# Optimization experiments

Hardware: AMD Instinct MI355X
Metric: run time of the kernel (lower is better)

Reference implementation:

```python
import jax, jax.numpy as jnp
import numpy as np

N_NODES = 50000
N_EDGES = 800000
D_IN = 128
D_HID = 128
N_CLASSES = 10


def setup_inputs() -> dict:
    key = jax.random.key(0)
    ks = jax.random.split(key, 8)
    x = jax.random.normal(ks[0], (N_NODES, D_IN), dtype=jnp.float32)
    edge_index = jax.random.randint(ks[1], (2, N_EDGES), 0, N_NODES, dtype=jnp.int64)
    s = 1.0 / np.sqrt(D_IN)
    W1 = jax.random.uniform(ks[2], (D_IN, D_HID), jnp.float32, -s, s)
    b1 = jnp.zeros((D_HID,), jnp.float32)
    W2 = jax.random.uniform(ks[3], (D_HID, D_HID), jnp.float32, -s, s)
    b2 = jnp.zeros((D_HID,), jnp.float32)
    sl = 1.0 / np.sqrt(D_HID)
    Wl = jax.random.uniform(ks[4], (D_HID, N_CLASSES), jnp.float32, -sl, sl)
    bl = jax.random.uniform(ks[5], (N_CLASSES,), jnp.float32, -sl, sl)
    return {"x": x, "edge_index": edge_index, "W1": W1, "b1": b1,
            "W2": W2, "b2": b2, "Wl": Wl, "bl": bl}


def gcn_conv(x, src, dst, W, b, n_nodes):
    # PyG GCNConv: add self-loops, symmetric normalization, gather-scatter aggregate
    h = x @ W                                             # [N, D_out]
    loop = jnp.arange(n_nodes, dtype=src.dtype)
    src2 = jnp.concatenate([src, loop])                   # [E+N]
    dst2 = jnp.concatenate([dst, loop])
    deg = jax.ops.segment_sum(jnp.ones_like(dst2, dtype=h.dtype), dst2,
                              num_segments=n_nodes)       # in-degree incl. self-loop
    dinv = jnp.where(deg > 0, jax.lax.rsqrt(deg), 0.0)
    norm = dinv[src2] * dinv[dst2]                        # [E+N]
    msgs = h[src2] * norm[:, None]                        # gather + scale  [E+N, D_out]
    out = jax.ops.segment_sum(msgs, dst2, num_segments=n_nodes)  # scatter-add
    return out + b


def reference(x, edge_index, W1, b1, W2, b2, Wl, bl):
    src, dst = edge_index[0], edge_index[1]
    n = x.shape[0]
    h = jax.nn.relu(gcn_conv(x, src, dst, W1, b1, n))     # dropout is identity in eval
    h = jax.nn.relu(gcn_conv(h, src, dst, W2, b2, n))
    logits = h @ Wl + bl                                  # [N, C]
    return jax.nn.log_softmax(logits, axis=1)
```

## Files before the change

kernel.cpp:

```cpp
#include <hip/hip_runtime.h>
#include <hip/hip_bf16.h>

#define D 128
#define NCLS 10

typedef short bf16x8 __attribute__((ext_vector_type(8)));
typedef float f32x4 __attribute__((ext_vector_type(4)));

static __device__ __forceinline__ float relu(float x){ return fmaxf(x, 0.0f); }
static __device__ __forceinline__ float bf_lo(unsigned v){ return __uint_as_float(v << 16); }
static __device__ __forceinline__ float bf_hi(unsigned v){ return __uint_as_float(v & 0xffff0000u); }
static __device__ __forceinline__ ushort bf16u(float f){
  __hip_bfloat16 h = __float2bfloat16(f);
  return *reinterpret_cast<ushort*>(&h);
}
static __device__ __forceinline__ unsigned relu_bf2(unsigned v){
  if (v & 0x00008000u) v &= 0xFFFF0000u;
  if (v & 0x80000000u) v &= 0x0000FFFFu;
  return v;
}

__global__ __launch_bounds__(256) void k_init(int* __restrict__ counts2, int nz,
                                              const float* __restrict__ W1,
                                              const float* __restrict__ W2,
                                              ushort* __restrict__ Wt1,
                                              ushort* __restrict__ Wt2){
  const int nzb = (nz + 255) >> 8;
  const int b = blockIdx.x;
  if (b < nzb){
    int i = b*256 + threadIdx.x;
    if (i < nz) counts2[i] = 0;
  } else {
    int i = (b - nzb)*256 + threadIdx.x;
    int sel = i >> 14;
    int rem = i & 16383;
    int k = rem >> 7, n = rem & 127;
    const float* Ws = sel ? W2 : W1;
    ushort* Wd = sel ? Wt2 : Wt1;
    Wd[n*128 + k] = bf16u(Ws[rem]);
  }
}

__global__ __launch_bounds__(256) void k_hist(const int* __restrict__ dst,
                                              int* __restrict__ counts, int E){
  int i = blockIdx.x*256 + threadIdx.x;
  int e0 = 2*i;
  if (e0 + 1 < E){
    int2 d = ((const int2*)dst)[i];
    atomicAdd(counts + d.x, 1);
    atomicAdd(counts + d.y, 1);
  } else if (e0 < E){
    atomicAdd(counts + dst[e0], 1);
  }
}

__global__ __launch_bounds__(256) void k_scan1(const int* __restrict__ counts,
                                               int2* __restrict__ rowPtr2,
                                               int* __restrict__ bsum,
                                               float* __restrict__ dinv, int n){
  const int i = blockIdx.x*256 + threadIdx.x;
  const int lane = threadIdx.x & 63;
  const int wid  = threadIdx.x >> 6;
  int v = (i < n) ? counts[i] : 0;
  if (i < n) dinv[i] = rsqrtf((float)(v + 1));
  int s = v;
  #pragma unroll
  for (int off = 1; off < 64; off <<= 1){
    int u = __shfl_up(s, off, 64);
    if (lane >= off) s += u;
  }
  __shared__ int ws[4];
  if (lane == 63) ws[wid] = s;
  __syncthreads();
  int add = 0;
  if (wid >= 1) add += ws[0];
  if (wid >= 2) add += ws[1];
  if (wid >= 3) add += ws[2];
  int incl = s + add;
  if (i < n) rowPtr2[i] = make_int2(incl - v, incl);
  if (threadIdx.x == 255) bsum[blockIdx.x] = incl;
}

__global__ __launch_bounds__(256) void k_scan2(int* __restrict__ bsum, int nb){
  const int t = threadIdx.x;
  const int lane = t & 63;
  const int wid  = t >> 6;
  int v = (t < nb) ? bsum[t] : 0;
  int s = v;
  #pragma unroll
  for (int off = 1; off < 64; off <<= 1){
    int u = __shfl_up(s, off, 64);
    if (lane >= off) s += u;
  }
  __shared__ int ws[4];
  if (lane == 63) ws[wid] = s;
  __syncthreads();
  int add = 0;
  if (wid >= 1) add += ws[0];
  if (wid >= 2) add += ws[1];
  if (wid >= 3) add += ws[2];
  int incl = s + add;
  if (t < nb) bsum[t] = incl - v;
}

__global__ __launch_bounds__(256) void k_scatter(const int* __restrict__ src,
                                                 const int* __restrict__ dst,
                                                 const int2* __restrict__ rowPtr2,
                                                 const int* __restrict__ bsum,
                                                 const float* __restrict__ dinv,
                                                 int* __restrict__ cursor,
                                                 int2* __restrict__ edat, int E){
  int i = blockIdx.x*256 + threadIdx.x;
  if (i >= E) return;
  int d = dst[i];
  int s = src[i];
  int pos = rowPtr2[d].x + bsum[d >> 8] + atomicAdd(cursor + d, 1);
  edat[pos] = make_int2(s, __float_as_int(dinv[s]));
}

template<bool BF16IN, bool RELU>
__global__ __launch_bounds__(256) void k_gemm_mfma(const void* __restrict__ Av,
                                                   const ushort* __restrict__ Wt,
                                                   __hip_bfloat16* __restrict__ C,
                                                   int M){
  __shared__ ushort sA[64*136];
  __shared__ ushort sW[128*136];
  const int tid = threadIdx.x;
  const int row0 = blockIdx.x * 64;
  const int rowsHere = (M - row0 >= 64) ? 64 : (M - row0);

  {
    const uint4* Wt4 = (const uint4*)Wt;
    for (int i = tid; i < 2048; i += 256){
      int r = i >> 4, c = i & 15;
      uint4 v = Wt4[i];
      *((uint4*)(sW + r*136 + c*8)) = v;
    }
  }
  if (BF16IN){
    const uint4* A4 = (const uint4*)((const ushort*)Av + (size_t)row0 * D);
    for (int i = tid; i < 64*16; i += 256){
      int r = i >> 4, c = i & 15;
      uint4 v = make_uint4(0,0,0,0);
      if (r < rowsHere) v = A4[i];
      if (RELU){ v.x = relu_bf2(v.x); v.y = relu_bf2(v.y);
                 v.z = relu_bf2(v.z); v.w = relu_bf2(v.w); }
      *((uint4*)(sA + r*136 + c*8)) = v;
    }
  } else {
    const float4* A4 = (const float4*)Av + (size_t)row0 * 32;
    for (int i = tid; i < 64*32; i += 256){
      int r = i >> 5, c = i & 31;
      float4 v = make_float4(0.f,0.f,0.f,0.f);
      if (r < rowsHere) v = A4[i];
      if (RELU){ v.x=relu(v.x); v.y=relu(v.y); v.z=relu(v.z); v.w=relu(v.w); }
      ushort4 p;
      p.x = bf16u(v.x); p.y = bf16u(v.y); p.z = bf16u(v.z); p.w = bf16u(v.w);
      *((ushort4*)(sA + r*136 + c*4)) = p;
    }
  }
  __syncthreads();

  const int wid  = tid >> 6;
  const int lane = tid & 63;
  const int fr = lane & 15;
  const int fq = lane >> 4;
  const ushort* aBase = sA + (wid*16 + fr)*136 + fq*8;
  const ushort* wBase = sW + fr*136 + fq*8;

  f32x4 acc0 = {0.f,0.f,0.f,0.f}, acc1 = acc0, acc2 = acc0, acc3 = acc0;
  f32x4 acc4 = acc0, acc5 = acc0, acc6 = acc0, acc7 = acc0;
  #pragma unroll
  for (int ks = 0; ks < 4; ++ks){
    bf16x8 a = *(const bf16x8*)(aBase + ks*32);
    bf16x8 b;
    b = *(const bf16x8*)(wBase + 0*16*136 + ks*32);
    acc0 = __builtin_amdgcn_mfma_f32_16x16x32_bf16(a, b, acc0, 0, 0, 0);
    b = *(const bf16x8*)(wBase + 1*16*136 + ks*32);
    acc1 = __builtin_amdgcn_mfma_f32_16x16x32_bf16(a, b, acc1, 0, 0, 0);
    b = *(const bf16x8*)(wBase + 2*16*136 + ks*32);
    acc2 = __builtin_amdgcn_mfma_f32_16x16x32_bf16(a, b, acc2, 0, 0, 0);
    b = *(const bf16x8*)(wBase + 3*16*136 + ks*32);
    acc3 = __builtin_amdgcn_mfma_f32_16x16x32_bf16(a, b, acc3, 0, 0, 0);
    b = *(const bf16x8*)(wBase + 4*16*136 + ks*32);
    acc4 = __builtin_amdgcn_mfma_f32_16x16x32_bf16(a, b, acc4, 0, 0, 0);
    b = *(const bf16x8*)(wBase + 5*16*136 + ks*32);
    acc5 = __builtin_amdgcn_mfma_f32_16x16x32_bf16(a, b, acc5, 0, 0, 0);
    b = *(const bf16x8*)(wBase + 6*16*136 + ks*32);
    acc6 = __builtin_amdgcn_mfma_f32_16x16x32_bf16(a, b, acc6, 0, 0, 0);
    b = *(const bf16x8*)(wBase + 7*16*136 + ks*32);
    acc7 = __builtin_amdgcn_mfma_f32_16x16x32_bf16(a, b, acc7, 0, 0, 0);
  }

  const int rbase = row0 + wid*16 + fq*4;
  #pragma unroll
  for (int r = 0; r < 4; ++r){
    int row = rbase + r;
    if (row < M){
      __hip_bfloat16* crow = C + (size_t)row*D + fr;
      crow[0*16]  = __float2bfloat16(acc0[r]);
      crow[1*16]  = __float2bfloat16(acc1[r]);
      crow[2*16]  = __float2bfloat16(acc2[r]);
      crow[3*16]  = __float2bfloat16(acc3[r]);
      crow[4*16]  = __float2bfloat16(acc4[r]);
      crow[5*16]  = __float2bfloat16(acc5[r]);
      crow[6*16]  = __float2bfloat16(acc6[r]);
      crow[7*16]  = __float2bfloat16(acc7[r]);
    }
  }
}

#define AGG_CORE_BF16                                                          \
  const int grp = lane >> 4;                                                   \
  const int q   = lane & 15;                                                   \
  float dn = dinv[node];                                                       \
  float4 aA0 = make_float4(0,0,0,0), aB0 = aA0, aA1 = aA0, aB1 = aA0;          \
  int2 be = rowPtr2[node];                                                     \
  int bs = bsum[node >> 8];                                                    \
  int beg = be.x + bs, end = be.y + bs;                                        \
  for (int j = beg; j < end; j += 64){                                         \
    int rem = end - j;                                                         \
    int cnt = (rem < 64) ? rem : 64;                                           \
    int2 ed = make_int2(0, 0);                                                 \
    if (lane < cnt) ed = edat[j + lane];                                       \
    int T = (((cnt + 3) >> 2) + 1) & ~1;                                       \
    for (int t = 0; t < T; t += 2){                                            \
      _Pragma("unroll")                                                        \
      for (int u = 0; u < 2; ++u){                                             \
        int e = 4*(t+u) + grp;                                                 \
        int sb = __shfl(ed.x, e);                                              \
        float nb = __uint_as_float((unsigned)__shfl(ed.y, e)) * dn;            \
        uint4 hv = ((const uint4*)(h + (size_t)sb*D))[q];                      \
        float4& cA = u ? aA1 : aA0;                                            \
        float4& cB = u ? aB1 : aB0;                                            \
        cA.x += bf_lo(hv.x)*nb; cA.y += bf_hi(hv.x)*nb;                        \
        cA.z += bf_lo(hv.y)*nb; cA.w += bf_hi(hv.y)*nb;                        \
        cB.x += bf_lo(hv.z)*nb; cB.y += bf_hi(hv.z)*nb;                        \
        cB.z += bf_lo(hv.w)*nb; cB.w += bf_hi(hv.w)*nb;                        \
      }                                                                        \
    }                                                                          \
  }                                                                            \
  float4 rA, rB;                                                               \
  rA.x=aA0.x+aA1.x; rA.y=aA0.y+aA1.y; rA.z=aA0.z+aA1.z; rA.w=aA0.w+aA1.w;      \
  rB.x=aB0.x+aB1.x; rB.y=aB0.y+aB1.y; rB.z=aB0.z+aB1.z; rB.w=aB0.w+aB1.w;      \
  rA.x += __shfl_xor(rA.x,16,64); rA.y += __shfl_xor(rA.y,16,64);              \
  rA.z += __shfl_xor(rA.z,16,64); rA.w += __shfl_xor(rA.w,16,64);              \
  rB.x += __shfl_xor(rB.x,16,64); rB.y += __shfl_xor(rB.y,16,64);              \
  rB.z += __shfl_xor(rB.z,16,64); rB.w += __shfl_xor(rB.w,16,64);              \
  rA.x += __shfl_xor(rA.x,32,64); rA.y += __shfl_xor(rA.y,32,64);              \
  rA.z += __shfl_xor(rA.z,32,64); rA.w += __shfl_xor(rA.w,32,64);              \
  rB.x += __shfl_xor(rB.x,32,64); rB.y += __shfl_xor(rB.y,32,64);              \
  rB.z += __shfl_xor(rB.z,32,64); rB.w += __shfl_xor(rB.w,32,64);

__global__ __launch_bounds__(256) void k_agg_csr(const ushort* __restrict__ h,
                                                 const int2* __restrict__ rowPtr2,
                                                 const int* __restrict__ bsum,
                                                 const int2* __restrict__ edat,
                                                 const float* __restrict__ dinv,
                                                 const float* __restrict__ b,
                                                 ushort* __restrict__ out, int n){
  int gid = blockIdx.x*256 + threadIdx.x;
  int node = gid >> 6;
  int lane = gid & 63;
  if (node >= n) return;
  AGG_CORE_BF16
  if (grp != 0) return;
  uint4 hs = ((const uint4*)(h + (size_t)node*D))[q];
  float sl = dn * dn;
  float4 bA = ((const float4*)b)[2*q];
  float4 bB = ((const float4*)b)[2*q + 1];
  float r[8];
  r[0] = rA.x + bf_lo(hs.x)*sl + bA.x;
  r[1] = rA.y + bf_hi(hs.x)*sl + bA.y;
  r[2] = rA.z + bf_lo(hs.y)*sl + bA.z;
  r[3] = rA.w + bf_hi(hs.y)*sl + bA.w;
  r[4] = rB.x + bf_lo(hs.z)*sl + bB.x;
  r[5] = rB.y + bf_hi(hs.z)*sl + bB.y;
  r[6] = rB.z + bf_lo(hs.w)*sl + bB.z;
  r[7] = rB.w + bf_hi(hs.w)*sl + bB.w;
  union Pack { uint4 u; __hip_bfloat16 b[8]; } p;
  #pragma unroll
  for (int i = 0; i < 8; ++i) p.b[i] = __float2bfloat16(r[i]);
  ((uint4*)(out + (size_t)node*D))[q] = p.u;
}

__global__ __launch_bounds__(256) void k_agg_head(const ushort* __restrict__ h,
                                                  const int2* __restrict__ rowPtr2,
                                                  const int* __restrict__ bsum,
                                                  const int2* __restrict__ edat,
                                                  const float* __restrict__ dinv,
                                                  const float* __restrict__ b,
                                                  const float* __restrict__ Wl,
                                                  const float* __restrict__ bl,
                                                  float* __restrict__ out, int n){
  int gid = blockIdx.x*256 + threadIdx.x;
  int node = gid >> 6;
  int lane = gid & 63;
  if (node >= n) return;
  AGG_CORE_BF16
  if (grp != 0) return;
  uint4 hs = ((const uint4*)(h + (size_t)node*D))[q];
  float sl = dn * dn;
  float4 bA = ((const float4*)b)[2*q];
  float4 bB = ((const float4*)b)[2*q + 1];
  float r[8];
  r[0] = relu(rA.x + bf_lo(hs.x)*sl + bA.x);
  r[1] = relu(rA.y + bf_hi(hs.x)*sl + bA.y);
  r[2] = relu(rA.z + bf_lo(hs.y)*sl + bA.z);
  r[3] = relu(rA.w + bf_hi(hs.y)*sl + bA.w);
  r[4] = relu(rB.x + bf_lo(hs.z)*sl + bB.x);
  r[5] = relu(rB.y + bf_hi(hs.z)*sl + bB.y);
  r[6] = relu(rB.z + bf_lo(hs.w)*sl + bB.z);
  r[7] = relu(rB.w + bf_hi(hs.w)*sl + bB.w);
  float lacc[NCLS];
  #pragma unroll
  for (int c = 0; c < NCLS; ++c){
    float a = 0.f;
    #pragma unroll
    for (int i = 0; i < 8; ++i) a += r[i] * Wl[(8*q + i)*NCLS + c];
    lacc[c] = a;
  }
  #pragma unroll
  for (int c = 0; c < NCLS; ++c){
    #pragma unroll
    for (int off = 8; off >= 1; off >>= 1)
      lacc[c] += __shfl_xor(lacc[c], off, 16);
    lacc[c] += bl[c];
  }
  float m = lacc[0];
  #pragma unroll
  for (int c = 1; c < NCLS; ++c) m = fmaxf(m, lacc[c]);
  float se = 0.f;
  #pragma unroll
  for (int c = 0; c < NCLS; ++c) se += expf(lacc[c] - m);
  float lse = m + logf(se);
  if (q < NCLS){
    float v = lacc[0];
    #pragma unroll
    for (int c = 1; c < NCLS; ++c) if (q == c) v = lacc[c];
    out[(size_t)node*NCLS + q] = v - lse;
  }
}

extern "C" void kernel_launch(void* const* d_in, const int* in_sizes, int n_in,
                              void* d_out, int out_size, void* d_ws, size_t ws_size,
                              hipStream_t stream){
  const float* x  = (const float*)d_in[0];
  const int*   ei = (const int*)d_in[1];
  const float* W1 = (const float*)d_in[2];
  const float* b1 = (const float*)d_in[3];
  const float* W2 = (const float*)d_in[4];
  const float* b2 = (const float*)d_in[5];
  const float* Wl = (const float*)d_in[6];
  const float* bl = (const float*)d_in[7];
  float* out = (float*)d_out;

  const int N = in_sizes[0] / D;
  const int E = in_sizes[1] / 2;
  const int* src = ei;
  const int* dst = ei + E;

  char* ws = (char*)d_ws;
  size_t off = 0;
  ushort* h1    = (ushort*)(ws + off); off += (size_t)N*D*2;
  ushort* g1    = (ushort*)(ws + off); off += (size_t)N*D*2;
  ushort* h2    = (ushort*)(ws + off); off += (size_t)N*D*2;
  ushort* Wt1   = (ushort*)(ws + off); off += (size_t)128*128*2;
  ushort* Wt2   = (ushort*)(ws + off); off += (size_t)128*128*2;
  int*   counts = (int*)(ws + off);    off += (size_t)N*4;
  int*   cursor = (int*)(ws + off);    off += (size_t)N*4;
  int2*  rowPtr2= (int2*)(ws + off);   off += (size_t)N*8;
  float* dinv   = (float*)(ws + off);  off += (size_t)N*4;
  int*   bsum   = (int*)(ws + off);    off += (size_t)256*4;
  int2*  edat   = (int2*)(ws + off);   off += (size_t)E*8;

  const int nbN   = (N + 255)/256;
  const int nb2N  = (2*N + 255)/256;
  const int nbE   = (E + 255)/256;
  const int nbE2  = (E/2 + 255)/256;
  const int initB = nb2N + 128;
  const int gemmB = (N + 63)/64;
  const int aggB  = (N + 3)/4;

  k_init<<<initB, 256, 0, stream>>>(counts, 2*N, W1, W2, Wt1, Wt2);
  k_hist<<<nbE2, 256, 0, stream>>>(dst, counts, E);
  k_scan1<<<nbN, 256, 0, stream>>>(counts, rowPtr2, bsum, dinv, N);
  k_scan2<<<1, 256, 0, stream>>>(bsum, nbN);
  k_scatter<<<nbE, 256, 0, stream>>>(src, dst, rowPtr2, bsum, dinv, cursor, edat, E);

  k_gemm_mfma<false,false><<<gemmB, 256, 0, stream>>>(x, Wt1, (__hip_bfloat16*)h1, N);
  k_agg_csr<<<aggB, 256, 0, stream>>>(h1, rowPtr2, bsum, edat, dinv, b1, g1, N);

  k_gemm_mfma<true,true><<<gemmB, 256, 0, stream>>>(g1, Wt2, (__hip_bfloat16*)h2, N);
  k_agg_head<<<aggB, 256, 0, stream>>>(h2, rowPtr2, bsum, edat, dinv, b2, Wl, bl, out, N);
}
```

Before: 207.5 us.

## Stage gathered neighbor rows into LDS via global_load_lds in aggregation

```diff
diff --git a/kernel.cpp b/kernel.cpp
--- a/kernel.cpp
+++ b/kernel.cpp
@@ -6,6 +6,12 @@
 
 typedef short bf16x8 __attribute__((ext_vector_type(8)));
 typedef float f32x4 __attribute__((ext_vector_type(4)));
+
+typedef __attribute__((address_space(1))) const unsigned int gas_u32;
+typedef __attribute__((address_space(3))) unsigned int las_u32;
+static __device__ __forceinline__ void gload16(const ushort* g, ushort* l){
+  __builtin_amdgcn_global_load_lds((gas_u32*)g, (las_u32*)l, 16, 0, 0);
+}
 
 static __device__ __forceinline__ float relu(float x){ return fmaxf(x, 0.0f); }
 static __device__ __forceinline__ float bf_lo(unsigned v){ return __uint_as_float(v << 16); }
@@ -210,47 +216,47 @@
   }
 }
 
-#define AGG_CORE_BF16                                                          \
-  const int grp = lane >> 4;                                                   \
-  const int q   = lane & 15;                                                   \
+#define AGG_CORE_STAGED                                                        \
+  const int wv   = threadIdx.x >> 6;                                           \
+  const int grp  = lane >> 4;                                                  \
+  const int q    = lane & 15;                                                  \
+  ushort* rowsW = sRows + wv*(32*128);                                         \
+  float*  normW = sNorm + wv*32;                                               \
   float dn = dinv[node];                                                       \
-  float4 aA0 = make_float4(0,0,0,0), aB0 = aA0, aA1 = aA0, aB1 = aA0;          \
+  float accx = 0.f, accy = 0.f;                                                \
   int2 be = rowPtr2[node];                                                     \
   int bs = bsum[node >> 8];                                                    \
   int beg = be.x + bs, end = be.y + bs;                                        \
-  for (int j = beg; j < end; j += 64){                                         \
+  for (int j = beg; j < end; j += 32){                                         \
     int rem = end - j;                                                         \
-    int cnt = (rem < 64) ? rem : 64;                                           \
+    int cnt = (rem < 32) ? rem : 32;                                           \
     int2 ed = make_int2(0, 0);                                                 \
-    if (lane < cnt) ed = edat[j + lane];                                       \
-    int T = (((cnt + 3) >> 2) + 1) & ~1;                                       \
-    for (int t = 0; t < T; t += 2){                                            \
+    float nf = 0.f;                                                            \
+    if (lane < cnt){                                                           \
+      ed = edat[j + lane];                                                     \
+      nf = __uint_as_float((unsigned)ed.y) * dn;                               \
+    }                                                                          \
+    if (lane < 32) normW[lane] = nf;                                           \
+    _Pragma("unroll")                                                          \
+    for (int i = 0; i < 8; ++i){                                               \
+      int e = i*4 + grp;                                                       \
+      e = (e < cnt) ? e : (cnt - 1);                                           \
+      int sb = __shfl(ed.x, e, 64);                                            \
+      gload16(h + ((size_t)sb << 7) + q*8, rowsW + i*512);                     \
+    }                                                                          \
+    asm volatile("s_waitcnt vmcnt(0)" ::: "memory");                           \
+    int T = (cnt + 3) >> 2;                                                    \
+    for (int t = 0; t < T; ++t){                                               \
       _Pragma("unroll")                                                        \
-      for (int u = 0; u < 2; ++u){                                             \
-        int e = 4*(t+u) + grp;                                                 \
-        int sb = __shfl(ed.x, e);                                              \
-        float nb = __uint_as_float((unsigned)__shfl(ed.y, e)) * dn;            \
-        uint4 hv = ((const uint4*)(h + (size_t)sb*D))[q];                      \
-        float4& cA = u ? aA1 : aA0;                                            \
-        float4& cB = u ? aB1 : aB0;                                            \
-        cA.x += bf_lo(hv.x)*nb; cA.y += bf_hi(hv.x)*nb;                        \
-        cA.z += bf_lo(hv.y)*nb; cA.w += bf_hi(hv.y)*nb;                        \
-        cB.x += bf_lo(hv.z)*nb; cB.y += bf_hi(hv.z)*nb;                        \
-        cB.z += bf_lo(hv.w)*nb; cB.w += bf_hi(hv.w)*nb;                        \
+      for (int u = 0; u < 4; ++u){                                             \
+        int k = t*4 + u;                                                       \
+        float nb = normW[k];                                                   \
+        unsigned hv = *(const unsigned*)(rowsW + k*128 + lane*2);              \
+        accx += bf_lo(hv)*nb;                                                  \
+        accy += bf_hi(hv)*nb;                                                  \
       }                                                                        \
     }                                                                          \
-  }                                                                            \
-  float4 rA, rB;                                                               \
-  rA.x=aA0.x+aA1.x; rA.y=aA0.y+aA1.y; rA.z=aA0.z+aA1.z; rA.w=aA0.w+aA1.w;      \
-  rB.x=aB0.x+aB1.x; rB.y=aB0.y+aB1.y; rB.z=aB0.z+aB1.z; rB.w=aB0.w+aB1.w;      \
-  rA.x += __shfl_xor(rA.x,16,64); rA.y += __shfl_xor(rA.y,16,64);              \
-  rA.z += __shfl_xor(rA.z,16,64); rA.w += __shfl_xor(rA.w,16,64);              \
-  rB.x += __shfl_xor(rB.x,16,64); rB.y += __shfl_xor(rB.y,16,64);              \
-  rB.z += __shfl_xor(rB.z,16,64); rB.w += __shfl_xor(rB.w,16,64);              \
-  rA.x += __shfl_xor(rA.x,32,64); rA.y += __shfl_xor(rA.y,32,64);              \
-  rA.z += __shfl_xor(rA.z,32,64); rA.w += __shfl_xor(rA.w,32,64);              \
-  rB.x += __shfl_xor(rB.x,32,64); rB.y += __shfl_xor(rB.y,32,64);              \
-  rB.z += __shfl_xor(rB.z,32,64); rB.w += __shfl_xor(rB.w,32,64);
+  }
 
 __global__ __launch_bounds__(256) void k_agg_csr(const ushort* __restrict__ h,
                                                  const int2* __restrict__ rowPtr2,
@@ -259,29 +265,19 @@
                                                  const float* __restrict__ dinv,
                                                  const float* __restrict__ b,
                                                  ushort* __restrict__ out, int n){
-  int gid = blockIdx.x*256 + threadIdx.x;
-  int node = gid >> 6;
-  int lane = gid & 63;
+  __shared__ ushort sRows[4*32*128];
+  __shared__ float  sNorm[4*32];
+  int node = blockIdx.x*4 + (threadIdx.x >> 6);
+  int lane = threadIdx.x & 63;
   if (node >= n) return;
-  AGG_CORE_BF16
-  if (grp != 0) return;
-  uint4 hs = ((const uint4*)(h + (size_t)node*D))[q];
+  AGG_CORE_STAGED
+  unsigned hs = *(const unsigned*)(h + ((size_t)node << 7) + lane*2);
+  float2 bv = ((const float2*)b)[lane];
   float sl = dn * dn;
-  float4 bA = ((const float4*)b)[2*q];
-  float4 bB = ((const float4*)b)[2*q + 1];
-  float r[8];
-  r[0] = rA.x + bf_lo(hs.x)*sl + bA.x;
-  r[1] = rA.y + bf_hi(hs.x)*sl + bA.y;
-  r[2] = rA.z + bf_lo(hs.y)*sl + bA.z;
-  r[3] = rA.w + bf_hi(hs.y)*sl + bA.w;
-  r[4] = rB.x + bf_lo(hs.z)*sl + bB.x;
-  r[5] = rB.y + bf_hi(hs.z)*sl + bB.y;
-  r[6] = rB.z + bf_lo(hs.w)*sl + bB.z;
-  r[7] = rB.w + bf_hi(hs.w)*sl + bB.w;
-  union Pack { uint4 u; __hip_bfloat16 b[8]; } p;
-  #pragma unroll
-  for (int i = 0; i < 8; ++i) p.b[i] = __float2bfloat16(r[i]);
-  ((uint4*)(out + (size_t)node*D))[q] = p.u;
+  float r0 = accx + bf_lo(hs)*sl + bv.x;
+  float r1 = accy + bf_hi(hs)*sl + bv.y;
+  unsigned po = ((unsigned)bf16u(r1) << 16) | (unsigned)bf16u(r0);
+  *(unsigned*)(out + ((size_t)node << 7) + lane*2) = po;
 }
 
 __global__ __launch_bounds__(256) void k_agg_head(const ushort* __restrict__ h,
@@ -293,38 +289,27 @@
                                                   const float* __restrict__ Wl,
                                                   const float* __restrict__ bl,
                                                   float* __restrict__ out, int n){
-  int gid = blockIdx.x*256 + threadIdx.x;
-  int node = gid >> 6;
-  int lane = gid & 63;
+  __shared__ ushort sRows[4*32*128];
+  __shared__ float  sNorm[4*32];
+  int node = blockIdx.x*4 + (threadIdx.x >> 6);
+  int lane = threadIdx.x & 63;
   if (node >= n) return;
-  AGG_CORE_BF16
-  if (grp != 0) return;
-  uint4 hs = ((const uint4*)(h + (size_t)node*D))[q];
+  AGG_CORE_STAGED
+  unsigned hs = *(const unsigned*)(h + ((size_t)node << 7) + lane*2);
+  float2 bv = ((const float2*)b)[lane];
   float sl = dn * dn;
-  float4 bA = ((const float4*)b)[2*q];
-  float4 bB = ((const float4*)b)[2*q + 1];
-  float r[8];
-  r[0] = relu(rA.x + bf_lo(hs.x)*sl + bA.x);
-  r[1] = relu(rA.y + bf_hi(hs.x)*sl + bA.y);
-  r[2] = relu(rA.z + bf_lo(hs.y)*sl + bA.z);
-  r[3] = relu(rA.w + bf_hi(hs.y)*sl + bA.w);
-  r[4] = relu(rB.x + bf_lo(hs.z)*sl + bB.x);
-  r[5] = relu(rB.y + bf_hi(hs.z)*sl + bB.y);
-  r[6] = relu(rB.z + bf_lo(hs.w)*sl + bB.z);
-  r[7] = relu(rB.w + bf_hi(hs.w)*sl + bB.w);
+  float r0 = relu(accx + bf_lo(hs)*sl + bv.x);
+  float r1 = relu(accy + bf_hi(hs)*sl + bv.y);
+  const float* wl0 = Wl + (2*lane)*NCLS;
   float lacc[NCLS];
   #pragma unroll
-  for (int c = 0; c < NCLS; ++c){
-    float a = 0.f;
-    #pragma unroll
-    for (int i = 0; i < 8; ++i) a += r[i] * Wl[(8*q + i)*NCLS + c];
-    lacc[c] = a;
-  }
+  for (int c = 0; c < NCLS; ++c)
+    lacc[c] = r0 * wl0[c] + r1 * wl0[NCLS + c];
   #pragma unroll
   for (int c = 0; c < NCLS; ++c){
     #pragma unroll
-    for (int off = 8; off >= 1; off >>= 1)
-      lacc[c] += __shfl_xor(lacc[c], off, 16);
+    for (int off = 32; off >= 1; off >>= 1)
+      lacc[c] += __shfl_xor(lacc[c], off, 64);
     lacc[c] += bl[c];
   }
   float m = lacc[0];
@@ -334,11 +319,11 @@
   #pragma unroll
   for (int c = 0; c < NCLS; ++c) se += expf(lacc[c] - m);
   float lse = m + logf(se);
-  if (q < NCLS){
+  if (lane < NCLS){
     float v = lacc[0];
     #pragma unroll
-    for (int c = 1; c < NCLS; ++c) if (q == c) v = lacc[c];
-    out[(size_t)node*NCLS + q] = v - lse;
+    for (int c = 1; c < NCLS; ++c) if (lane == c) v = lacc[c];
+    out[(size_t)node*NCLS + lane] = v - lse;
   }
 }
 
```

Result: slower. 217.3 us (+4.8%).
